# Performance work log

Hardware: AMD Instinct MI355X
Metric: run time of the kernel (lower is better)

Reference implementation:

```python
import jax, jax.numpy as jnp
import numpy as np

SLOPE = 25.0  # snntorch surrogate.fast_sigmoid default slope

@jax.custom_vjp
def fast_sigmoid(x):
    # Forward: Heaviside step (spike); backward: fast-sigmoid surrogate grad.
    return (x > 0).astype(x.dtype)

def _fs_fwd(x):
    return fast_sigmoid(x), x

def _fs_bwd(x, g):
    return (g / (SLOPE * jnp.abs(x) + 1.0) ** 2,)

fast_sigmoid.defvjp(_fs_fwd, _fs_bwd)


def setup_inputs() -> dict:
    key = jax.random.key(0)
    k0, k1, k2, k3, k4 = jax.random.split(key, 5)
    B, IN, OUT, T = 512, 512, 512, 64
    x = jax.random.normal(k0, (B, IN), jnp.float32)
    W = jax.random.normal(k1, (OUT, IN), jnp.float32) / np.sqrt(IN).astype(np.float32)
    b = jnp.zeros((OUT,), jnp.float32)
    # learnable scalars (0.0 in source init; small nonzero to exercise the P recurrence)
    alpha = jax.random.uniform(k2, (1,), jnp.float32) * 0.1
    eta = jax.random.uniform(k3, (1,), jnp.float32) * 0.01
    beta = jax.random.uniform(k4, (1,), jnp.float32) * 0.1
    P0 = jnp.zeros((OUT, IN), jnp.float32)
    return {"x": x, "W": W, "b": b, "alpha": alpha, "eta": eta, "beta": beta, "P0": P0, "T": T}


def reference(x, W, b, alpha, eta, beta, P0, T):
    # x: [B, IN], W: [OUT, IN], P0: [OUT, IN]
    tao_u, tao_w, dt, V_th = 5.0, 1.0, 1.0, 0.2
    k = jnp.float32(dt / tao_u)
    a = alpha.reshape(())
    e = eta.reshape(())
    bt = beta.reshape(())
    # MLP output is constant across timesteps (same s_batch each step)
    mlp_T = jax.nn.relu(x @ W.T + b).T  # [OUT, B]
    xT = x.T  # [IN, B]
    decay_p = jnp.exp(jnp.float32(-dt / tao_w))

    # NOTE: reset() zeroes u and s every step, so only P is recurrent:
    # u_m = k * (mlp_out * exp(-m/tao_w) + alpha * P @ x^T)
    def step(P, m):
        u = k * (mlp_T * jnp.exp(-m / tao_w) + a * (P @ xT))  # [OUT, B]
        P_new = P * decay_p + e * ((fast_sigmoid(u) + bt) @ x)  # [OUT, IN]
        s = fast_sigmoid(u - V_th)  # [OUT, B]
        return P_new, s.T  # emit [B, OUT]

    _, spk = jax.lax.scan(step, P0, jnp.arange(T, dtype=jnp.float32))
    return spk  # [T, B, OUT]
```

## Files before the change

kernel.cpp:

```cpp
#include <hip/hip_runtime.h>


#define NN 512

__global__ __launch_bounds__(256) void gemm_splitk_kernel(
    const float* __restrict__ x, const float* __restrict__ W,
    const float* __restrict__ P0, float* __restrict__ part)
{
    const int tid = threadIdx.x;
    const int bid = blockIdx.x;
    const int out = bid >> 8;
    const int rem = bid & 255;
    const int kq = rem >> 6;
    const int tl = rem & 63;
    const int rb = (tl >> 3) << 6;
    const int cb = (tl & 7) << 6;
    const int kbase = kq << 7;

    const float* A = ((out == 0) ? W : (out == 1) ? P0 : x) + (size_t)rb * NN;
    const float* Bx = x + (size_t)cb * NN;
    float* D = part + (size_t)(out * 4 + kq) * NN * NN;

    const int tx = tid & 15;
    const int ty = tid >> 4;

    __shared__ float At[32][68];
    __shared__ float Bt[32][68];

    const int lr = tid >> 2;
    const int lk = (tid & 3) << 3;

    float acc[4][4] = {{0.f,0.f,0.f,0.f},{0.f,0.f,0.f,0.f},
                       {0.f,0.f,0.f,0.f},{0.f,0.f,0.f,0.f}};

    float4 a0 = *(const float4*)(A + (size_t)lr * NN + kbase + lk);
    float4 a1 = *(const float4*)(A + (size_t)lr * NN + kbase + lk + 4);
    float4 b0 = *(const float4*)(Bx + (size_t)lr * NN + kbase + lk);
    float4 b1 = *(const float4*)(Bx + (size_t)lr * NN + kbase + lk + 4);

    for (int c = 0; c < 4; ++c) {
        __syncthreads();
        At[lk + 0][lr] = a0.x; At[lk + 1][lr] = a0.y;
        At[lk + 2][lr] = a0.z; At[lk + 3][lr] = a0.w;
        At[lk + 4][lr] = a1.x; At[lk + 5][lr] = a1.y;
        At[lk + 6][lr] = a1.z; At[lk + 7][lr] = a1.w;
        Bt[lk + 0][lr] = b0.x; Bt[lk + 1][lr] = b0.y;
        Bt[lk + 2][lr] = b0.z; Bt[lk + 3][lr] = b0.w;
        Bt[lk + 4][lr] = b1.x; Bt[lk + 5][lr] = b1.y;
        Bt[lk + 6][lr] = b1.z; Bt[lk + 7][lr] = b1.w;
        __syncthreads();

        if (c < 3) {
            const int k0 = kbase + ((c + 1) << 5);
            a0 = *(const float4*)(A + (size_t)lr * NN + k0 + lk);
            a1 = *(const float4*)(A + (size_t)lr * NN + k0 + lk + 4);
            b0 = *(const float4*)(Bx + (size_t)lr * NN + k0 + lk);
            b1 = *(const float4*)(Bx + (size_t)lr * NN + k0 + lk + 4);
        }

#pragma unroll
        for (int k = 0; k < 32; ++k) {
            const float4 av = *(const float4*)&At[k][4 * ty];
            const float4 bv = *(const float4*)&Bt[k][4 * tx];
            const float avs[4] = {av.x, av.y, av.z, av.w};
            const float bvs[4] = {bv.x, bv.y, bv.z, bv.w};
#pragma unroll
            for (int i = 0; i < 4; ++i)
#pragma unroll
                for (int j = 0; j < 4; ++j)
                    acc[i][j] = fmaf(avs[i], bvs[j], acc[i][j]);
        }
    }

#pragma unroll
    for (int i = 0; i < 4; ++i) {
        const int r = rb + 4 * ty + i;
        *(float4*)(D + (size_t)r * NN + cb + 4 * tx) =
            make_float4(acc[i][0], acc[i][1], acc[i][2], acc[i][3]);
    }
}

__global__ __launch_bounds__(256) void combine_kernel(
    const float* __restrict__ part, const float* __restrict__ bias,
    float* __restrict__ M, float* __restrict__ V0, float* __restrict__ G)
{
    const int idx = blockIdx.x * 256 + threadIdx.x;
    const int out = idx >> 16;
    const int io = idx & 65535;
    const float4* p = (const float4*)(part + (size_t)out * 4 * NN * NN);
    const float4 p0 = p[io];
    const float4 p1 = p[io + 65536];
    const float4 p2 = p[io + 131072];
    const float4 p3 = p[io + 196608];
    float4 s;
    s.x = (p0.x + p1.x) + (p2.x + p3.x);
    s.y = (p0.y + p1.y) + (p2.y + p3.y);
    s.z = (p0.z + p1.z) + (p2.z + p3.z);
    s.w = (p0.w + p1.w) + (p2.w + p3.w);
    if (out == 0) {
        const float bb = bias[io >> 7];
        s.x = fmaxf(s.x + bb, 0.f); s.y = fmaxf(s.y + bb, 0.f);
        s.z = fmaxf(s.z + bb, 0.f); s.w = fmaxf(s.w + bb, 0.f);
        ((float4*)M)[io] = s;
    } else if (out == 1) {
        ((float4*)V0)[io] = s;
    } else {
        ((float4*)G)[io] = s;
    }
}

__global__ __launch_bounds__(256) void acc0_splitk_kernel(
    const float* __restrict__ M, const float* __restrict__ V0,
    const float* __restrict__ G, const float* __restrict__ alpha,
    float* __restrict__ ACC0p, float* __restrict__ gsp)
{
    const int tid = threadIdx.x;
    const int bid = blockIdx.x;
    const int kq = bid >> 6;
    const int tl = bid & 63;
    const int rb = (tl >> 3) << 6;
    const int cb = (tl & 7) << 6;
    const int kbase = kq << 6;

    const float a = alpha[0];
    const float kk = 0.2f;

    const int tx = tid & 15;
    const int ty = tid >> 4;

    __shared__ float At[32][68];
    __shared__ float Bt[32][68];

    const int ar = tid >> 2;
    const int akk = (tid & 3) << 3;
    const int kb = tid >> 3;
    const int cl = (tid & 7) << 3;

    float acc[4][4] = {{0.f,0.f,0.f,0.f},{0.f,0.f,0.f,0.f},
                       {0.f,0.f,0.f,0.f},{0.f,0.f,0.f,0.f}};

    float4 m0 = *(const float4*)(M + (size_t)(rb + ar) * NN + kbase + akk);
    float4 m1 = *(const float4*)(M + (size_t)(rb + ar) * NN + kbase + akk + 4);
    float4 v0 = *(const float4*)(V0 + (size_t)(rb + ar) * NN + kbase + akk);
    float4 v1 = *(const float4*)(V0 + (size_t)(rb + ar) * NN + kbase + akk + 4);
    float4 g0 = *(const float4*)(G + (size_t)(kbase + kb) * NN + cb + cl);
    float4 g1 = *(const float4*)(G + (size_t)(kbase + kb) * NN + cb + cl + 4);

    for (int c = 0; c < 2; ++c) {
        __syncthreads();
        At[akk + 0][ar] = (kk * fmaf(a, v0.x, m0.x) > 0.f) ? 1.f : 0.f;
        At[akk + 1][ar] = (kk * fmaf(a, v0.y, m0.y) > 0.f) ? 1.f : 0.f;
        At[akk + 2][ar] = (kk * fmaf(a, v0.z, m0.z) > 0.f) ? 1.f : 0.f;
        At[akk + 3][ar] = (kk * fmaf(a, v0.w, m0.w) > 0.f) ? 1.f : 0.f;
        At[akk + 4][ar] = (kk * fmaf(a, v1.x, m1.x) > 0.f) ? 1.f : 0.f;
        At[akk + 5][ar] = (kk * fmaf(a, v1.y, m1.y) > 0.f) ? 1.f : 0.f;
        At[akk + 6][ar] = (kk * fmaf(a, v1.z, m1.z) > 0.f) ? 1.f : 0.f;
        At[akk + 7][ar] = (kk * fmaf(a, v1.w, m1.w) > 0.f) ? 1.f : 0.f;
        Bt[kb][cl + 0] = g0.x; Bt[kb][cl + 1] = g0.y;
        Bt[kb][cl + 2] = g0.z; Bt[kb][cl + 3] = g0.w;
        Bt[kb][cl + 4] = g1.x; Bt[kb][cl + 5] = g1.y;
        Bt[kb][cl + 6] = g1.z; Bt[kb][cl + 7] = g1.w;
        __syncthreads();

        if (c < 1) {
            const int k0 = kbase + 32;
            m0 = *(const float4*)(M + (size_t)(rb + ar) * NN + k0 + akk);
            m1 = *(const float4*)(M + (size_t)(rb + ar) * NN + k0 + akk + 4);
            v0 = *(const float4*)(V0 + (size_t)(rb + ar) * NN + k0 + akk);
            v1 = *(const float4*)(V0 + (size_t)(rb + ar) * NN + k0 + akk + 4);
            g0 = *(const float4*)(G + (size_t)(k0 + kb) * NN + cb + cl);
            g1 = *(const float4*)(G + (size_t)(k0 + kb) * NN + cb + cl + 4);
        }

#pragma unroll
        for (int k = 0; k < 32; ++k) {
            const float4 av = *(const float4*)&At[k][4 * ty];
            const float4 bv = *(const float4*)&Bt[k][4 * tx];
            const float avs[4] = {av.x, av.y, av.z, av.w};
            const float bvs[4] = {bv.x, bv.y, bv.z, bv.w};
#pragma unroll
            for (int i = 0; i < 4; ++i)
#pragma unroll
                for (int j = 0; j < 4; ++j)
                    acc[i][j] = fmaf(avs[i], bvs[j], acc[i][j]);
        }
    }

    float* Dp = ACC0p + (size_t)kq * NN * NN;
#pragma unroll
    for (int i = 0; i < 4; ++i) {
        *(float4*)(Dp + (size_t)(rb + 4 * ty + i) * NN + cb + 4 * tx) =
            make_float4(acc[i][0], acc[i][1], acc[i][2], acc[i][3]);
    }

    if ((tl >> 3) == 0) {
        __syncthreads();
        float* red = &At[0][0];
        const int c = cb + (tid & 63);
        const int g = tid >> 6;
        float s = 0.f;
#pragma unroll 16
        for (int i = 0; i < 16; ++i)
            s += G[(size_t)(kbase + 16 * g + i) * NN + c];
        red[g * 64 + (tid & 63)] = s;
        __syncthreads();
        if (g == 0) {
            const int cc = tid & 63;
            gsp[kq * NN + c] =
                (red[cc] + red[64 + cc]) + (red[128 + cc] + red[192 + cc]);
        }
    }
}

__global__ __launch_bounds__(512, 4) void snn_bits11_kernel(
    const float* __restrict__ M, const float* __restrict__ G,
    const float* __restrict__ V0, const float* __restrict__ ACC0p,
    const float* __restrict__ gsp, const float* __restrict__ alpha,
    const float* __restrict__ eta, const float* __restrict__ beta,
    unsigned* __restrict__ sp, int T)
{
    const int tid = threadIdx.x;
    const int w = tid >> 6;
    const int lane = tid & 63;
    const int r = blockIdx.x;

    __shared__ unsigned long long sbbuf[64][8];
    __shared__ unsigned long long lflag[2];
    __shared__ int wcnt[8];
    __shared__ unsigned short list[528] __attribute__((aligned(16)));

    const float a = alpha[0], e = eta[0], bt = beta[0];
    const float kk = 0.2f;
    const float dd = 0.36787944117144233f;
    const float Vth = 0.2f;

    const size_t rc = (size_t)r * NN + tid;
    const float m = M[rc];
    float v = V0[rc];
    const float gsum =
        ((gsp[tid] + gsp[NN + tid]) + (gsp[2 * NN + tid] + gsp[3 * NN + tid])) +
        ((gsp[4 * NN + tid] + gsp[5 * NN + tid]) + (gsp[6 * NN + tid] + gsp[7 * NN + tid]));
    const float cg = e * bt * gsum;
    const float* Gc = G + tid;

    float acc;
    float em;
    unsigned long long oldw;

    {
        const float u = kk * fmaf(a, v, m * 1.0f);
        const unsigned long long hb = __ballot(u > 0.f);
        const unsigned long long sb = __ballot(u > Vth);
        if (lane == 0) sbbuf[0][w] = sb;
        oldw = hb;
        const float* A0 = ACC0p + rc;
        const size_t S = (size_t)NN * NN;
        acc = ((A0[0] + A0[S]) + (A0[2 * S] + A0[3 * S]))
            + ((A0[4 * S] + A0[5 * S]) + (A0[6 * S] + A0[7 * S]));
        v = fmaf(dd, v, fmaf(e, acc, cg));
        em = dd;
    }

    for (int t = 1; t < T; ++t) {
        const float u = kk * fmaf(a, v, m * em);
        const unsigned long long hb = __ballot(u > 0.f);
        const unsigned long long sb = __ballot(u > Vth);
        const unsigned long long xw = hb ^ oldw;
        const int p = t & 1;
        if (lane == 0) {
            ((unsigned char*)&lflag[p])[w] = (xw != 0ull) ? (unsigned char)1 : (unsigned char)0;
            wcnt[w] = (int)__popcll(xw);
            sbbuf[t][w] = sb;
        }
        __syncthreads();

        if (lflag[p] != 0ull) {
            const int c0 = wcnt[0], c1 = wcnt[1], c2 = wcnt[2], c3 = wcnt[3];
            const int c4 = wcnt[4], c5 = wcnt[5], c6 = wcnt[6], c7 = wcnt[7];
            const int ntot = ((c0 + c1) + (c2 + c3)) + ((c4 + c5) + (c6 + c7));
            int base = 0;
            if (w > 0) base += c0;
            if (w > 1) base += c1;
            if (w > 2) base += c2;
            if (w > 3) base += c3;
            if (w > 4) base += c4;
            if (w > 5) base += c5;
            if (w > 6) base += c6;

            if ((xw >> lane) & 1ull) {
                const int pos = (int)__popcll(xw & ((1ull << lane) - 1ull));
                const unsigned row = (unsigned)((w << 6) + lane);
                const unsigned sgn = (unsigned)((hb >> lane) & 1ull) << 15;
                list[base + pos] = (unsigned short)(row | sgn);
            }
            __syncthreads();

            float s0 = 0.f, s1 = 0.f, s2 = 0.f, s3 = 0.f;
            float s4 = 0.f, s5 = 0.f, s6 = 0.f, s7 = 0.f;
            for (int j = 0; j < ntot; j += 8) {
                const uint4 le = *(const uint4*)(list + j);
                const unsigned e0 = le.x & 0xFFFFu, e1 = le.x >> 16;
                const unsigned e2 = le.y & 0xFFFFu, e3 = le.y >> 16;
                const unsigned e4 = le.z & 0xFFFFu, e5 = le.z >> 16;
                const unsigned e6 = le.w & 0xFFFFu, e7 = le.w >> 16;
                const float g0 = Gc[(size_t)(e0 & 511u) << 9];
                const float g1 = Gc[(size_t)(e1 & 511u) << 9];
                const float g2 = Gc[(size_t)(e2 & 511u) << 9];
                const float g3 = Gc[(size_t)(e3 & 511u) << 9];
                const float g4 = Gc[(size_t)(e4 & 511u) << 9];
                const float g5 = Gc[(size_t)(e5 & 511u) << 9];
                const float g6 = Gc[(size_t)(e6 & 511u) << 9];
                const float g7 = Gc[(size_t)(e7 & 511u) << 9];
                s0 += (j + 0 < ntot) ? ((e0 & 0x8000u) ? g0 : -g0) : 0.0f;
                s1 += (j + 1 < ntot) ? ((e1 & 0x8000u) ? g1 : -g1) : 0.0f;
                s2 += (j + 2 < ntot) ? ((e2 & 0x8000u) ? g2 : -g2) : 0.0f;
                s3 += (j + 3 < ntot) ? ((e3 & 0x8000u) ? g3 : -g3) : 0.0f;
                s4 += (j + 4 < ntot) ? ((e4 & 0x8000u) ? g4 : -g4) : 0.0f;
                s5 += (j + 5 < ntot) ? ((e5 & 0x8000u) ? g5 : -g5) : 0.0f;
                s6 += (j + 6 < ntot) ? ((e6 & 0x8000u) ? g6 : -g6) : 0.0f;
                s7 += (j + 7 < ntot) ? ((e7 & 0x8000u) ? g7 : -g7) : 0.0f;
            }
            acc += ((s0 + s1) + (s2 + s3)) + ((s4 + s5) + (s6 + s7));
        }

        oldw = hb;
        v = fmaf(dd, v, fmaf(e, acc, cg));
        em *= dd;
    }

    __syncthreads();
    const unsigned* sbw = (const unsigned*)&sbbuf[0][0];
    for (int idx = tid; idx < T * 16; idx += 512) {
        const int t = idx >> 4;
        const int word = idx & 15;
        sp[(size_t)t * (NN * 16) + (size_t)r * 16 + word] = sbw[t * 16 + word];
    }
}

__global__ __launch_bounds__(256) void expand_kernel(
    const unsigned* __restrict__ sp, float* __restrict__ out)
{
    const int tid = threadIdx.x;
    const int t = blockIdx.x >> 3;
    const int bt8 = blockIdx.x & 7;

    __shared__ uint2 sh[NN];
    const uint2* spw = (const uint2*)sp;
    sh[tid]       = spw[((size_t)t * NN + tid) * 8 + bt8];
    sh[tid + 256] = spw[((size_t)t * NN + tid + 256) * 8 + bt8];
    __syncthreads();

    const int b = bt8 * 64 + (tid >> 2);
    const int sub = tid & 3;
    const int rw = (tid >> 2) >> 5;
    const int bit = b & 31;
    float* op = out + (size_t)t * (NN * NN) + (size_t)b * NN;

#pragma unroll 4
    for (int i = 0; i < 32; ++i) {
        const int o = sub * 4 + i * 16;
        const uint2 w0 = sh[o];
        const uint2 w1 = sh[o + 1];
        const uint2 w2 = sh[o + 2];
        const uint2 w3 = sh[o + 3];
        float4 f;
        f.x = (float)(((rw ? w0.y : w0.x) >> bit) & 1u);
        f.y = (float)(((rw ? w1.y : w1.x) >> bit) & 1u);
        f.z = (float)(((rw ? w2.y : w2.x) >> bit) & 1u);
        f.w = (float)(((rw ? w3.y : w3.x) >> bit) & 1u);
        *(float4*)(op + o) = f;
    }
}

__global__ __launch_bounds__(256) void gemm64_kernel(
    const float* __restrict__ x, const float* __restrict__ W,
    const float* __restrict__ P0, const float* __restrict__ bias,
    float* __restrict__ M, float* __restrict__ V0, float* __restrict__ G)
{
    const int tid = threadIdx.x;
    const int bid = blockIdx.x;
    const int out = bid >> 6;
    const int tl = bid & 63;
    const int rb = (tl >> 3) << 6;
    const int cb = (tl & 7) << 6;

    const float* A = ((out == 0) ? W : (out == 1) ? P0 : x) + (size_t)rb * NN;
    const float* Bx = x + (size_t)cb * NN;
    float* D = (out == 0) ? M : (out == 1) ? V0 : G;

    const int tx = tid & 15;
    const int ty = tid >> 4;

    __shared__ float At[32][68];
    __shared__ float Bt[32][68];

    const int lr = tid >> 2;
    const int lk = (tid & 3) << 3;

    float acc[4][4] = {{0.f,0.f,0.f,0.f},{0.f,0.f,0.f,0.f},
                       {0.f,0.f,0.f,0.f},{0.f,0.f,0.f,0.f}};

    float4 a0 = *(const float4*)(A + (size_t)lr * NN + lk);
    float4 a1 = *(const float4*)(A + (size_t)lr * NN + lk + 4);
    float4 b0 = *(const float4*)(Bx + (size_t)lr * NN + lk);
    float4 b1 = *(const float4*)(Bx + (size_t)lr * NN + lk + 4);

    for (int c = 0; c < 16; ++c) {
        __syncthreads();
        At[lk + 0][lr] = a0.x; At[lk + 1][lr] = a0.y;
        At[lk + 2][lr] = a0.z; At[lk + 3][lr] = a0.w;
        At[lk + 4][lr] = a1.x; At[lk + 5][lr] = a1.y;
        At[lk + 6][lr] = a1.z; At[lk + 7][lr] = a1.w;
        Bt[lk + 0][lr] = b0.x; Bt[lk + 1][lr] = b0.y;
        Bt[lk + 2][lr] = b0.z; Bt[lk + 3][lr] = b0.w;
        Bt[lk + 4][lr] = b1.x; Bt[lk + 5][lr] = b1.y;
        Bt[lk + 6][lr] = b1.z; Bt[lk + 7][lr] = b1.w;
        __syncthreads();

        if (c < 15) {
            const int k0 = (c + 1) << 5;
            a0 = *(const float4*)(A + (size_t)lr * NN + k0 + lk);
            a1 = *(const float4*)(A + (size_t)lr * NN + k0 + lk + 4);
            b0 = *(const float4*)(Bx + (size_t)lr * NN + k0 + lk);
            b1 = *(const float4*)(Bx + (size_t)lr * NN + k0 + lk + 4);
        }

#pragma unroll
        for (int k = 0; k < 32; ++k) {
            const float4 av = *(const float4*)&At[k][4 * ty];
            const float4 bv = *(const float4*)&Bt[k][4 * tx];
            const float avs[4] = {av.x, av.y, av.z, av.w};
            const float bvs[4] = {bv.x, bv.y, bv.z, bv.w};
#pragma unroll
            for (int i = 0; i < 4; ++i)
#pragma unroll
                for (int j = 0; j < 4; ++j)
                    acc[i][j] = fmaf(avs[i], bvs[j], acc[i][j]);
        }
    }

#pragma unroll
    for (int i = 0; i < 4; ++i) {
        const int r = rb + 4 * ty + i;
        float4 o = make_float4(acc[i][0], acc[i][1], acc[i][2], acc[i][3]);
        if (out == 0) {
            const float bb = bias[r];
            o.x = fmaxf(o.x + bb, 0.f); o.y = fmaxf(o.y + bb, 0.f);
            o.z = fmaxf(o.z + bb, 0.f); o.w = fmaxf(o.w + bb, 0.f);
        }
        *(float4*)(D + (size_t)r * NN + cb + 4 * tx) = o;
    }
}

__global__ __launch_bounds__(256) void colsum_kernel(
    const float* __restrict__ G, float* __restrict__ gs)
{
    __shared__ float red[4][64];
    const int tid = threadIdx.x;
    const int c = (blockIdx.x << 6) + (tid & 63);
    const int g = tid >> 6;
    float s = 0.f;
#pragma unroll 8
    for (int bp = 128 * g; bp < 128 * g + 128; ++bp) s += G[(size_t)bp * NN + c];
    if (g > 0) red[g][tid & 63] = s;
    __syncthreads();
    if (g == 0) gs[c] = ((s + red[1][tid & 63]) + red[2][tid & 63]) + red[3][tid & 63];
}

__global__ __launch_bounds__(256) void snn_step_kernel(
    const float* __restrict__ M, const float* __restrict__ G,
    const float* __restrict__ V0, const float* __restrict__ gs,
    const float* __restrict__ alpha, const float* __restrict__ eta,
    const float* __restrict__ beta, float* __restrict__ out, int T)
{
    const int j = threadIdx.x;
    const int r0 = blockIdx.x * 2;
    const int c0 = 2 * j;
    const float a = alpha[0], e = eta[0], bt = beta[0];
    const float kk = 0.2f, dd = 0.36787944117144233f, Vth = 0.2f;

    float v00 = V0[r0 * NN + c0];
    float v01 = V0[r0 * NN + c0 + 1];
    float v10 = V0[(r0 + 1) * NN + c0];
    float v11 = V0[(r0 + 1) * NN + c0 + 1];
    const float m00 = M[r0 * NN + c0];
    const float m01 = M[r0 * NN + c0 + 1];
    const float m10 = M[(r0 + 1) * NN + c0];
    const float m11 = M[(r0 + 1) * NN + c0 + 1];
    const float gs0 = gs[c0];
    const float gs1 = gs[c0 + 1];

    __shared__ float2 hp[NN];
    float em = 1.0f;
    const float2* Gcol = (const float2*)G + j;

    for (int t = 0; t < T; ++t) {
        const float u00 = kk * (m00 * em + a * v00);
        const float u01 = kk * (m01 * em + a * v01);
        const float u10 = kk * (m10 * em + a * v10);
        const float u11 = kk * (m11 * em + a * v11);

        float* outp = out + (size_t)t * (NN * NN);
        float2 sA = make_float2(u00 > Vth ? 1.f : 0.f, u10 > Vth ? 1.f : 0.f);
        float2 sB = make_float2(u01 > Vth ? 1.f : 0.f, u11 > Vth ? 1.f : 0.f);
        *(float2*)(outp + (size_t)c0 * NN + r0) = sA;
        *(float2*)(outp + (size_t)(c0 + 1) * NN + r0) = sB;

        hp[c0]     = make_float2(u00 > 0.f ? 1.f : 0.f, u10 > 0.f ? 1.f : 0.f);
        hp[c0 + 1] = make_float2(u01 > 0.f ? 1.f : 0.f, u11 > 0.f ? 1.f : 0.f);
        __syncthreads();

        float acc00 = 0.f, acc01 = 0.f, acc10 = 0.f, acc11 = 0.f;
#pragma unroll 8
        for (int bp = 0; bp < NN; ++bp) {
            float2 h = hp[bp];
            float2 g = Gcol[(size_t)bp * 256];
            acc00 = fmaf(h.x, g.x, acc00);
            acc01 = fmaf(h.x, g.y, acc01);
            acc10 = fmaf(h.y, g.x, acc10);
            acc11 = fmaf(h.y, g.y, acc11);
        }

        v00 = dd * v00 + e * (acc00 + bt * gs0);
        v01 = dd * v01 + e * (acc01 + bt * gs1);
        v10 = dd * v10 + e * (acc10 + bt * gs0);
        v11 = dd * v11 + e * (acc11 + bt * gs1);
        em *= dd;
        __syncthreads();
    }
}

extern "C" void kernel_launch(void* const* d_in, const int* in_sizes, int n_in,
                              void* d_out, int out_size, void* d_ws, size_t ws_size,
                              hipStream_t stream)
{
    const float* x     = (const float*)d_in[0];
    const float* W     = (const float*)d_in[1];
    const float* bias  = (const float*)d_in[2];
    const float* alpha = (const float*)d_in[3];
    const float* eta   = (const float*)d_in[4];
    const float* beta  = (const float*)d_in[5];
    const float* P0    = (const float*)d_in[6];
    (void)in_sizes; (void)n_in;

    const int T = out_size / (NN * NN);

    float* ws    = (float*)d_ws;
    float* part  = ws;
    float* ACC0p = ws;
    float* M     = ws + 12 * NN * NN;
    float* V0    = ws + 13 * NN * NN;
    float* G     = ws + 14 * NN * NN;
    float* gsp   = ws + 15 * NN * NN;
    unsigned* sp = (unsigned*)(gsp + 8 * NN);

    const size_t need_main = ((size_t)15 * NN * NN + 8 * NN) * 4
                             + (size_t)T * NN * 16 * 4;

    if (ws_size >= need_main && T <= 64) {
        hipLaunchKernelGGL(gemm_splitk_kernel, dim3(768), dim3(256), 0, stream,
                           x, W, P0, part);
        hipLaunchKernelGGL(combine_kernel, dim3(768), dim3(256), 0, stream,
                           part, bias, M, V0, G);
        hipLaunchKernelGGL(acc0_splitk_kernel, dim3(512), dim3(256), 0, stream,
                           M, V0, G, alpha, ACC0p, gsp);
        hipLaunchKernelGGL(snn_bits11_kernel, dim3(NN), dim3(512), 0, stream,
                           M, G, V0, ACC0p, gsp, alpha, eta, beta, sp, T);
        hipLaunchKernelGGL(expand_kernel, dim3(T * 8), dim3(256), 0, stream,
                           sp, (float*)d_out);
    } else {
        float* Mf  = ws;
        float* V0f = ws + NN * NN;
        float* Gf  = ws + 2 * NN * NN;
        float* gs2 = ws + 3 * NN * NN;
        hipLaunchKernelGGL(gemm64_kernel, dim3(192), dim3(256), 0, stream,
                           x, W, P0, bias, Mf, V0f, Gf);
        hipLaunchKernelGGL(colsum_kernel, dim3(8), dim3(256), 0, stream, Gf, gs2);
        hipLaunchKernelGGL(snn_step_kernel, dim3(256), dim3(256), 0, stream,
                           Mf, Gf, V0f, gs2, alpha, eta, beta, (float*)d_out, T);
    }
}
```

Before: 109.6 us.

## Fuse split-K combine into acc0 GEMM and pack per-wave counts into one word

Removes the separate combine kernel by having the acc0 GEMM read the four split-K partials directly, rebuild M, V0 and G on the fly, and write those arrays from a subset of blocks. This drops one kernel launch and one round trip of M/V0/G through global memory, but each block now rereads partials redundantly and the workspace grows to hold ACC0p separately. In the SNN step kernel, per-wave flip counts are packed as bytes into one 64-bit shared word, replacing the separate flag and count arrays so a single load serves both checks. The old path stays as a fallback when the workspace is too small.

```diff
diff --git a/kernel.cpp b/kernel.cpp
--- a/kernel.cpp
+++ b/kernel.cpp
@@ -77,6 +77,139 @@
         const int r = rb + 4 * ty + i;
         *(float4*)(D + (size_t)r * NN + cb + 4 * tx) =
             make_float4(acc[i][0], acc[i][1], acc[i][2], acc[i][3]);
+    }
+}
+
+__global__ __launch_bounds__(256) void acc0_fused_kernel(
+    const float* __restrict__ part, const float* __restrict__ bias,
+    const float* __restrict__ alpha, float* __restrict__ ACC0p,
+    float* __restrict__ gsp, float* __restrict__ M,
+    float* __restrict__ V0, float* __restrict__ G)
+{
+    const int tid = threadIdx.x;
+    const int bid = blockIdx.x;
+    const int kq = bid >> 6;
+    const int tl = bid & 63;
+    const int rb = (tl >> 3) << 6;
+    const int cb = (tl & 7) << 6;
+    const int kbase = kq << 6;
+
+    const float a = alpha[0];
+    const float kk = 0.2f;
+    const size_t S = (size_t)NN * NN;
+    const float* Mp = part;
+    const float* Vp = part + 4 * S;
+    const float* Gp = part + 8 * S;
+
+    const int tx = tid & 15;
+    const int ty = tid >> 4;
+
+    __shared__ float At[32][68];
+    __shared__ float Bt[32][68];
+
+    const int ar = tid >> 2;
+    const int akk = (tid & 3) << 3;
+    const int kb = tid >> 3;
+    const int cl = (tid & 7) << 3;
+
+    const float bb = bias[rb + ar];
+    const bool wMV = ((tl & 7) == 0);
+    const bool wG  = ((tl >> 3) == 0);
+
+    float acc[4][4] = {{0.f,0.f,0.f,0.f},{0.f,0.f,0.f,0.f},
+                       {0.f,0.f,0.f,0.f},{0.f,0.f,0.f,0.f}};
+
+    for (int c = 0; c < 2; ++c) {
+        const int kpos = kbase + (c << 5);
+        __syncthreads();
+#pragma unroll
+        for (int hx = 0; hx < 2; ++hx) {
+            const int off = akk + 4 * hx;
+            const size_t ai = (size_t)(rb + ar) * NN + kpos + off;
+            const float4 m0 = *(const float4*)(Mp + ai);
+            const float4 m1 = *(const float4*)(Mp + S + ai);
+            const float4 m2 = *(const float4*)(Mp + 2 * S + ai);
+            const float4 m3 = *(const float4*)(Mp + 3 * S + ai);
+            const float4 w0 = *(const float4*)(Vp + ai);
+            const float4 w1 = *(const float4*)(Vp + S + ai);
+            const float4 w2 = *(const float4*)(Vp + 2 * S + ai);
+            const float4 w3 = *(const float4*)(Vp + 3 * S + ai);
+            float4 vs, mf;
+            vs.x = (w0.x + w1.x) + (w2.x + w3.x);
+            vs.y = (w0.y + w1.y) + (w2.y + w3.y);
+            vs.z = (w0.z + w1.z) + (w2.z + w3.z);
+            vs.w = (w0.w + w1.w) + (w2.w + w3.w);
+            mf.x = fmaxf(((m0.x + m1.x) + (m2.x + m3.x)) + bb, 0.f);
+            mf.y = fmaxf(((m0.y + m1.y) + (m2.y + m3.y)) + bb, 0.f);
+            mf.z = fmaxf(((m0.z + m1.z) + (m2.z + m3.z)) + bb, 0.f);
+            mf.w = fmaxf(((m0.w + m1.w) + (m2.w + m3.w)) + bb, 0.f);
+            At[off + 0][ar] = (kk * fmaf(a, vs.x, mf.x) > 0.f) ? 1.f : 0.f;
+            At[off + 1][ar] = (kk * fmaf(a, vs.y, mf.y) > 0.f) ? 1.f : 0.f;
+            At[off + 2][ar] = (kk * fmaf(a, vs.z, mf.z) > 0.f) ? 1.f : 0.f;
+            At[off + 3][ar] = (kk * fmaf(a, vs.w, mf.w) > 0.f) ? 1.f : 0.f;
+            if (wMV) {
+                *(float4*)(M + ai) = mf;
+                *(float4*)(V0 + ai) = vs;
+            }
+        }
+#pragma unroll
+        for (int hx = 0; hx < 2; ++hx) {
+            const int off = cl + 4 * hx;
+            const size_t gi = (size_t)(kpos + kb) * NN + cb + off;
+            const float4 g0 = *(const float4*)(Gp + gi);
+            const float4 g1 = *(const float4*)(Gp + S + gi);
+            const float4 g2 = *(const float4*)(Gp + 2 * S + gi);
+            const float4 g3 = *(const float4*)(Gp + 3 * S + gi);
+            float4 gs;
+            gs.x = (g0.x + g1.x) + (g2.x + g3.x);
+            gs.y = (g0.y + g1.y) + (g2.y + g3.y);
+            gs.z = (g0.z + g1.z) + (g2.z + g3.z);
+            gs.w = (g0.w + g1.w) + (g2.w + g3.w);
+            Bt[kb][off + 0] = gs.x; Bt[kb][off + 1] = gs.y;
+            Bt[kb][off + 2] = gs.z; Bt[kb][off + 3] = gs.w;
+            if (wG) *(float4*)(G + gi) = gs;
+        }
+        __syncthreads();
+
+#pragma unroll
+        for (int k = 0; k < 32; ++k) {
+            const float4 av = *(const float4*)&At[k][4 * ty];
+            const float4 bv = *(const float4*)&Bt[k][4 * tx];
+            const float avs[4] = {av.x, av.y, av.z, av.w};
+            const float bvs[4] = {bv.x, bv.y, bv.z, bv.w};
+#pragma unroll
+            for (int i = 0; i < 4; ++i)
+#pragma unroll
+                for (int j = 0; j < 4; ++j)
+                    acc[i][j] = fmaf(avs[i], bvs[j], acc[i][j]);
+        }
+    }
+
+    float* Dp = ACC0p + (size_t)kq * S;
+#pragma unroll
+    for (int i = 0; i < 4; ++i) {
+        *(float4*)(Dp + (size_t)(rb + 4 * ty + i) * NN + cb + 4 * tx) =
+            make_float4(acc[i][0], acc[i][1], acc[i][2], acc[i][3]);
+    }
+
+    if (wG) {
+        __syncthreads();
+        float* red = &At[0][0];
+        const int c = cb + (tid & 63);
+        const int g = tid >> 6;
+        float s = 0.f;
+#pragma unroll 16
+        for (int i = 0; i < 16; ++i) {
+            const size_t ri = (size_t)(kbase + 16 * g + i) * NN + c;
+            s += ((Gp[ri] + Gp[S + ri]) + (Gp[2 * S + ri] + Gp[3 * S + ri]));
+        }
+        red[g * 64 + (tid & 63)] = s;
+        __syncthreads();
+        if (g == 0) {
+            const int cc = tid & 63;
+            gsp[kq * NN + c] =
+                (red[cc] + red[64 + cc]) + (red[128 + cc] + red[192 + cc]);
+        }
     }
 }
 
@@ -212,7 +345,7 @@
     }
 }
 
-__global__ __launch_bounds__(512, 4) void snn_bits11_kernel(
+__global__ __launch_bounds__(512, 4) void snn_bits12_kernel(
     const float* __restrict__ M, const float* __restrict__ G,
     const float* __restrict__ V0, const float* __restrict__ ACC0p,
     const float* __restrict__ gsp, const float* __restrict__ alpha,
@@ -225,8 +358,7 @@
     const int r = blockIdx.x;
 
     __shared__ unsigned long long sbbuf[64][8];
-    __shared__ unsigned long long lflag[2];
-    __shared__ int wcnt[8];
+    __shared__ unsigned long long wcw[2];
     __shared__ unsigned short list[528] __attribute__((aligned(16)));
 
     const float a = alpha[0], e = eta[0], bt = beta[0];
@@ -268,15 +400,21 @@
         const unsigned long long xw = hb ^ oldw;
         const int p = t & 1;
         if (lane == 0) {
-            ((unsigned char*)&lflag[p])[w] = (xw != 0ull) ? (unsigned char)1 : (unsigned char)0;
-            wcnt[w] = (int)__popcll(xw);
+            ((unsigned char*)&wcw[p])[w] = (unsigned char)__popcll(xw);
             sbbuf[t][w] = sb;
         }
         __syncthreads();
 
-        if (lflag[p] != 0ull) {
-            const int c0 = wcnt[0], c1 = wcnt[1], c2 = wcnt[2], c3 = wcnt[3];
-            const int c4 = wcnt[4], c5 = wcnt[5], c6 = wcnt[6], c7 = wcnt[7];
+        const unsigned long long cw = wcw[p];
+        if (cw != 0ull) {
+            const int c0 = (int)(cw & 255u);
+            const int c1 = (int)((cw >> 8) & 255u);
+            const int c2 = (int)((cw >> 16) & 255u);
+            const int c3 = (int)((cw >> 24) & 255u);
+            const int c4 = (int)((cw >> 32) & 255u);
+            const int c5 = (int)((cw >> 40) & 255u);
+            const int c6 = (int)((cw >> 48) & 255u);
+            const int c7 = (int)((cw >> 56) & 255u);
             const int ntot = ((c0 + c1) + (c2 + c3)) + ((c4 + c5) + (c6 + c7));
             int base = 0;
             if (w > 0) base += c0;
@@ -544,35 +682,54 @@
     (void)in_sizes; (void)n_in;
 
     const int T = out_size / (NN * NN);
-
-    float* ws    = (float*)d_ws;
-    float* part  = ws;
-    float* ACC0p = ws;
-    float* M     = ws + 12 * NN * NN;
-    float* V0    = ws + 13 * NN * NN;
-    float* G     = ws + 14 * NN * NN;
-    float* gsp   = ws + 15 * NN * NN;
-    unsigned* sp = (unsigned*)(gsp + 8 * NN);
-
-    const size_t need_main = ((size_t)15 * NN * NN + 8 * NN) * 4
-                             + (size_t)T * NN * 16 * 4;
-
-    if (ws_size >= need_main && T <= 64) {
+    const size_t S = (size_t)NN * NN;
+    float* ws = (float*)d_ws;
+
+    const size_t spw = (size_t)T * NN * 16;
+    const size_t need_fused = (23 * S + 8 * NN) * 4 + spw * 4;
+    const size_t need_mid = (15 * S + 8 * NN) * 4 + spw * 4;
+
+    if (ws_size >= need_fused && T <= 64) {
+        float* part  = ws;
+        float* ACC0p = ws + 12 * S;
+        float* M     = ws + 20 * S;
+        float* V0    = ws + 21 * S;
+        float* G     = ws + 22 * S;
+        float* gsp   = ws + 23 * S;
+        unsigned* sp = (unsigned*)(gsp + 8 * NN);
+
+        hipLaunchKernelGGL(gemm_splitk_kernel, dim3(768), dim3(256), 0, stream,
+                           x, W, P0, part);
+        hipLaunchKernelGGL(acc0_fused_kernel, dim3(512), dim3(256), 0, stream,
+                           part, bias, alpha, ACC0p, gsp, M, V0, G);
+        hipLaunchKernelGGL(snn_bits12_kernel, dim3(NN), dim3(512), 0, stream,
+                           M, G, V0, ACC0p, gsp, alpha, eta, beta, sp, T);
+        hipLaunchKernelGGL(expand_kernel, dim3(T * 8), dim3(256), 0, stream,
+                           sp, (float*)d_out);
+    } else if (ws_size >= need_mid && T <= 64) {
+        float* part  = ws;
+        float* ACC0p = ws;
+        float* M     = ws + 12 * S;
+        float* V0    = ws + 13 * S;
+        float* G     = ws + 14 * S;
+        float* gsp   = ws + 15 * S;
+        unsigned* sp = (unsigned*)(gsp + 8 * NN);
+
         hipLaunchKernelGGL(gemm_splitk_kernel, dim3(768), dim3(256), 0, stream,
                            x, W, P0, part);
         hipLaunchKernelGGL(combine_kernel, dim3(768), dim3(256), 0, stream,
                            part, bias, M, V0, G);
         hipLaunchKernelGGL(acc0_splitk_kernel, dim3(512), dim3(256), 0, stream,
                            M, V0, G, alpha, ACC0p, gsp);
-        hipLaunchKernelGGL(snn_bits11_kernel, dim3(NN), dim3(512), 0, stream,
+        hipLaunchKernelGGL(snn_bits12_kernel, dim3(NN), dim3(512), 0, stream,
                            M, G, V0, ACC0p, gsp, alpha, eta, beta, sp, T);
         hipLaunchKernelGGL(expand_kernel, dim3(T * 8), dim3(256), 0, stream,
                            sp, (float*)d_out);
     } else {
         float* Mf  = ws;
-        float* V0f = ws + NN * NN;
-        float* Gf  = ws + 2 * NN * NN;
-        float* gs2 = ws + 3 * NN * NN;
+        float* V0f = ws + S;
+        float* Gf  = ws + 2 * S;
+        float* gs2 = ws + 3 * S;
         hipLaunchKernelGGL(gemm64_kernel, dim3(192), dim3(256), 0, stream,
                            x, W, P0, bias, Mf, V0f, Gf);
         hipLaunchKernelGGL(colsum_kernel, dim3(8), dim3(256), 0, stream, Gf, gs2);
```

After: 122.8 us. 1.12x slower.
